# Performance work log

Hardware: AMD Instinct MI355X
Metric: run time of the kernel (lower is better)

## Reference

```python
import jax, jax.numpy as jnp
import numpy as np

B, F_IN, N, S = 2, 128, 192, 192   # batch, in_features, n_nodes, seq (seq==n_nodes required by mask broadcast)
H, D = 4, 64                        # n_heads, n_hidden (out_features = H*D = 256)
NEG_SLOPE = 0.2


def setup_inputs() -> dict:
    key = jax.random.key(0)
    ks = jax.random.split(key, 6)
    X = jax.random.normal(ks[0], (B, F_IN, N, S), dtype=jnp.float32)
    A = jax.random.randint(ks[1], (N, N, 1), 0, 2, dtype=jnp.int32)
    W_lin = jax.random.normal(ks[2], (F_IN, H * D), dtype=jnp.float32) * 0.05
    b_lin = jax.random.uniform(ks[3], (H * D,), dtype=jnp.float32)
    W_attn = jax.random.normal(ks[4], (2 * D,), dtype=jnp.float32) * 0.05
    b_attn = jax.random.uniform(ks[5], (1,), dtype=jnp.float32)
    return {"X": X, "A": A, "W_lin": W_lin, "b_lin": b_lin,
            "W_attn": W_attn, "b_attn": b_attn}


def reference(X, A, W_lin, b_lin, W_attn, b_attn):
    # Dropout is identity (eval mode).
    b, f, n, s = X.shape
    x = jnp.transpose(X, (0, 3, 2, 1))                      # (b, s, n, f)
    g = (x @ W_lin + b_lin).reshape(b, s, n, H, D)          # (b, s, n, H, D)
    # attn is affine: attn(cat[g_i, g_j]) = a_src.g_i + a_dst.g_j + b_attn
    a_src, a_dst = W_attn[:D], W_attn[D:]
    s_src = jnp.einsum('bsnhd,d->bsnh', g, a_src)
    s_dst = jnp.einsum('bsnhd,d->bsnh', g, a_dst)
    e = s_src[:, :, :, None, :] + s_dst[:, :, None, :, :] + b_attn[0]  # (b, s, n_i, n_j, H)
    e = jnp.where(e >= 0, e, NEG_SLOPE * e)                 # LeakyReLU
    # torch masked_fill broadcast: mask (n,n,1,1) aligns with e dims (s, n_i, n_j, H)
    e = jnp.where(A[..., None] == 0, -jnp.inf, e)
    alphas = jax.nn.softmax(e, axis=1)                      # softmax over seq dim (dim=1, as in source)
    alphas = jnp.nan_to_num(alphas, nan=0.0)
    # einsum 'mnojh,klphf->mnohf': independent sums over j (alphas) and k,l,p (g)
    sum_g = g.sum(axis=(0, 1, 2))                           # (H, D)
    attn_res = alphas.sum(axis=3)[..., None] * sum_g        # (b, s, n, H, D)
    out = attn_res.reshape(b, s, n, H * D)                  # concat=True
    return jnp.transpose(out, (0, 3, 2, 1))                 # (b, out_features, n, s)
```

## Files before the change

### kernel.cpp

```cpp
#include <hip/hip_runtime.h>
#include <math.h>

#define B_ 2
#define F_ 128
#define N_ 192
#define S_ 192
#define NS_ (N_ * S_)
#define SLOPE 0.2f
#define LOG2E 1.4426950408889634f
#define NEG_INF (-__builtin_inff())

#if defined(__has_builtin)
#if __has_builtin(__builtin_amdgcn_exp2f)
#define EXP2(x) __builtin_amdgcn_exp2f(x)
#else
#define EXP2(x) exp2f(x)
#endif
#else
#define EXP2(x) exp2f(x)
#endif

#define OFF_WSRC 0
#define OFF_WDST 512
#define OFF_CSRC 1024
#define OFF_CDST 1028
#define OFF_SUMG 1040
#define OFF_PART 1296
#define OFF_PE   2320
#define OFF_QD   (OFF_PE + 8 * NS_ * 2)
#define OFF_QT   (OFF_QD + 8 * NS_ * 2)

__global__ __launch_bounds__(256) void kPre(const float* __restrict__ X,
                                            const float* __restrict__ W_lin,
                                            const float* __restrict__ b_lin,
                                            const float* __restrict__ W_attn,
                                            const float* __restrict__ b_attn,
                                            float* __restrict__ ws) {
    int blk = blockIdx.x, t = threadIdx.x;
    if (blk < 1024) {
        int sq = blk & 3, f = (blk >> 2) & 127, b = blk >> 9;
        const float4* p = (const float4*)(X + ((size_t)(b * F_ + f)) * NS_ + sq * 9216);
        float acc = 0.f;
#pragma unroll
        for (int k = 0; k < 9; k++) {
            float4 v = p[t + k * 256];
            acc += (v.x + v.y) + (v.z + v.w);
        }
        for (int o = 32; o; o >>= 1) acc += __shfl_down(acc, o, 64);
        __shared__ float red[4];
        if ((t & 63) == 0) red[t >> 6] = acc;
        __syncthreads();
        if (t == 0)
            ws[OFF_PART + sq * 256 + b * 128 + f] = (red[0] + red[1]) + (red[2] + red[3]);
    } else if (blk == 1024) {
        const float4* wa = (const float4*)W_attn;
        for (int c = t; c < 512; c += 256) {
            int f = c >> 2, h = c & 3;
            const float4* wl = (const float4*)(W_lin + f * 256 + h * 64);
            float as = 0.f, ad = 0.f;
#pragma unroll
            for (int q = 0; q < 16; q++) {
                float4 w = wl[q], a1 = wa[q], a2 = wa[16 + q];
                as += w.x * a1.x + w.y * a1.y + w.z * a1.z + w.w * a1.w;
                ad += w.x * a2.x + w.y * a2.y + w.z * a2.z + w.w * a2.w;
            }
            ws[OFF_WSRC + c] = as * LOG2E;
            ws[OFF_WDST + c] = ad * LOG2E;
        }
    } else {
        if (t < 4) {
            float c = 0.f;
            for (int d = 0; d < 64; d++) c += b_lin[t * 64 + d] * W_attn[d];
            ws[OFF_CSRC + t] = (c + b_attn[0]) * LOG2E;
        } else if (t < 8) {
            int h = t - 4;
            float c = 0.f;
            for (int d = 0; d < 64; d++) c += b_lin[h * 64 + d] * W_attn[64 + d];
            ws[OFF_CDST + h] = c * LOG2E;
        }
    }
}

__global__ __launch_bounds__(256) void kProj(const float* __restrict__ X,
                                             const int* __restrict__ A,
                                             const float* __restrict__ W_lin,
                                             const float* __restrict__ b_lin,
                                             float* __restrict__ ws) {
    __shared__ float4 wsl[128], wdl[128];
    __shared__ float red[4 * 64 * 9];
    __shared__ float xs[128];
    __shared__ float wbuf[4096];
    int t = threadIdx.x, blk = blockIdx.x;
    if (blk < 1152) {
        int n = blk % 192, bsc = blk / 192;
        int b = bsc / 3, sc = bsc % 3;
        if (t < 128) {
            wsl[t] = ((const float4*)(ws + OFF_WSRC))[t];
            wdl[t] = ((const float4*)(ws + OFF_WDST))[t];
        }
        __syncthreads();
        int fq = t >> 6, lane = t & 63;
        int s = sc * 64 + lane;
        float aS[4] = {0, 0, 0, 0}, aD[4] = {0, 0, 0, 0};
        const float* xp = X + (size_t)(b * F_) * NS_ + n * S_ + s;
        int f0 = fq * 32;
#pragma unroll 8
        for (int fi = 0; fi < 32; fi++) {
            float x = xp[(size_t)(f0 + fi) * NS_];
            float4 w1 = wsl[f0 + fi], w2 = wdl[f0 + fi];
            aS[0] += x * w1.x; aS[1] += x * w1.y; aS[2] += x * w1.z; aS[3] += x * w1.w;
            aD[0] += x * w2.x; aD[1] += x * w2.y; aD[2] += x * w2.z; aD[3] += x * w2.w;
        }
        float* rp = red + t * 9;
#pragma unroll
        for (int h = 0; h < 4; h++) { rp[h] = aS[h]; rp[4 + h] = aD[h]; }
        __syncthreads();
        float2* PEp = (float2*)(ws + OFF_PE);
        float2* QDp = (float2*)(ws + OFF_QD);
        float2* QTp = (float2*)(ws + OFF_QT);
#pragma unroll
        for (int c = t; c < 512; c += 256) {
            int s_loc = c >> 3, k = c & 7;
            float v = red[s_loc * 9 + k] + red[(64 + s_loc) * 9 + k] +
                      red[(128 + s_loc) * 9 + k] + red[(192 + s_loc) * 9 + k];
            int ss = sc * 64 + s_loc;
            if (k < 4) {
                int bh = b * 4 + k;
                bool masked = (A[ss * 192 + n] == 0);
                float2 pr;
                if (masked) { pr.x = 0.f; pr.y = 0.f; }
                else {
                    float pt = v + ws[OFF_CSRC + k];
                    pr.x = EXP2(pt); pr.y = EXP2(0.2f * pt);
                }
                PEp[(size_t)bh * NS_ + n * 192 + ss] = pr;
            } else {
                int h = k - 4, bh = b * 4 + h;
                float dv = v + ws[OFF_CDST + h];
                float2 qr; qr.x = EXP2(dv); qr.y = EXP2(0.2f * dv);
                QDp[(size_t)bh * NS_ + ss * 192 + n] = qr;
                QTp[(size_t)bh * NS_ + n * 192 + ss] = qr;
            }
        }
    } else {
        if (t < 128) {
            float v = 0.f;
#pragma unroll
            for (int q = 0; q < 8; q++) v += ws[OFF_PART + q * 128 + t];
            xs[t] = v;
        }
        float acc = 0.f;
        for (int ch = 0; ch < 8; ch++) {
            const float4* s4 = (const float4*)(W_lin + ch * 4096);
            __syncthreads();
#pragma unroll
            for (int k = 0; k < 4; k++) ((float4*)wbuf)[t + k * 256] = s4[t + k * 256];
            __syncthreads();
#pragma unroll
            for (int fi = 0; fi < 16; fi++) acc += xs[ch * 16 + fi] * wbuf[fi * 256 + t];
        }
        ws[OFF_SUMG + t] = acc + 73728.f * b_lin[t];
    }
}

__global__ __launch_bounds__(384) void kAttn(const float* __restrict__ ws,
                                             float* __restrict__ out) {
    int blk = blockIdx.x, t = threadIdx.x;
    int bh = blk & 7, iq = blk >> 3;
    int b = bh >> 2, h = bh & 3;
    __shared__ float4 pe4[192];
    __shared__ float zpart[768];
    __shared__ float zr_sh[384];
    __shared__ float sg_sh[64];
    const float2* PEp = (const float2*)(ws + OFF_PE) + (size_t)bh * NS_;
    const float2* QDp = (const float2*)(ws + OFF_QD) + (size_t)bh * NS_;
    const float2* QTp = (const float2*)(ws + OFF_QT) + (size_t)bh * NS_;
    if (t < 64) sg_sh[t] = ws[OFF_SUMG + h * 64 + t];
    if (t < 192) {
        float2 a = PEp[(iq * 2) * 192 + t];
        float2 c = PEp[(iq * 2 + 1) * 192 + t];
        pe4[t] = make_float4(a.x, a.y, c.x, c.y);
    }
    __syncthreads();

    {
        int sq = t / 192, j = t - sq * 192;
        float z0 = 0.f, z1 = 0.f;
#pragma unroll 8
        for (int s = sq * 96; s < sq * 96 + 96; s++) {
            float4 E = pe4[s];
            float2 F = QDp[s * 192 + j];
            z0 += fmaxf(E.x * F.x, E.y * F.y);
            z1 += fmaxf(E.z * F.x, E.w * F.y);
        }
        zpart[sq * 384 + j] = z0;
        zpart[sq * 384 + 192 + j] = z1;
    }
    __syncthreads();
    {
        float Z = zpart[t] + zpart[384 + t];
        zr_sh[t] = (Z != 0.f) ? (1.f / Z) : 0.f;
    }
    __syncthreads();

    {
        int i_loc = t / 192, s = t - i_loc * 192;
        float4 E4 = pe4[s];
        float Ex = i_loc ? E4.z : E4.x;
        float Ey = i_loc ? E4.w : E4.y;
        const float* zr = zr_sh + i_loc * 192;
        float acc = 0.f;
#pragma unroll 8
        for (int j = 0; j < 192; j++) {
            float2 G = QTp[j * 192 + s];
            acc += fmaxf(Ex * G.x, Ey * G.y) * zr[j];
        }
        int i = iq * 2 + i_loc;
        float* op = out + (((size_t)(b * 256 + h * 64)) * 192 + i) * 192 + s;
#pragma unroll 8
        for (int d = 0; d < 64; d++)
            op[(size_t)d * NS_] = acc * sg_sh[d];
    }
}

extern "C" void kernel_launch(void* const* d_in, const int* in_sizes, int n_in,
                              void* d_out, int out_size, void* d_ws, size_t ws_size,
                              hipStream_t stream) {
    const float* X      = (const float*)d_in[0];
    const int*   A      = (const int*)d_in[1];
    const float* W_lin  = (const float*)d_in[2];
    const float* b_lin  = (const float*)d_in[3];
    const float* W_attn = (const float*)d_in[4];
    const float* b_attn = (const float*)d_in[5];
    float* out = (float*)d_out;
    float* ws  = (float*)d_ws;

    kPre<<<1026, 256, 0, stream>>>(X, W_lin, b_lin, W_attn, b_attn, ws);
    kProj<<<1153, 256, 0, stream>>>(X, A, W_lin, b_lin, ws);
    kAttn<<<768, 384, 0, stream>>>(ws, out);
}
```

Before: 159.8 us.

## Store raw dst scores and recompute exponentials in attention, three rows per block

```diff
diff --git a/kernel.cpp b/kernel.cpp
--- a/kernel.cpp
+++ b/kernel.cpp
@@ -28,7 +28,7 @@
 #define OFF_PART 1296
 #define OFF_PE   2320
 #define OFF_QD   (OFF_PE + 8 * NS_ * 2)
-#define OFF_QT   (OFF_QD + 8 * NS_ * 2)
+#define OFF_QT   (OFF_QD + 8 * NS_)
 
 __global__ __launch_bounds__(256) void kPre(const float* __restrict__ X,
                                             const float* __restrict__ W_lin,
@@ -116,8 +116,8 @@
         for (int h = 0; h < 4; h++) { rp[h] = aS[h]; rp[4 + h] = aD[h]; }
         __syncthreads();
         float2* PEp = (float2*)(ws + OFF_PE);
-        float2* QDp = (float2*)(ws + OFF_QD);
-        float2* QTp = (float2*)(ws + OFF_QT);
+        float*  QDf = ws + OFF_QD;
+        float*  QTf = ws + OFF_QT;
 #pragma unroll
         for (int c = t; c < 512; c += 256) {
             int s_loc = c >> 3, k = c & 7;
@@ -137,9 +137,8 @@
             } else {
                 int h = k - 4, bh = b * 4 + h;
                 float dv = v + ws[OFF_CDST + h];
-                float2 qr; qr.x = EXP2(dv); qr.y = EXP2(0.2f * dv);
-                QDp[(size_t)bh * NS_ + ss * 192 + n] = qr;
-                QTp[(size_t)bh * NS_ + n * 192 + ss] = qr;
+                QDf[(size_t)bh * NS_ + ss * 192 + n] = dv;
+                QTf[(size_t)bh * NS_ + n * 192 + ss] = dv;
             }
         }
     } else {
@@ -163,59 +162,81 @@
     }
 }
 
-__global__ __launch_bounds__(384) void kAttn(const float* __restrict__ ws,
+__global__ __launch_bounds__(576) void kAttn(const float* __restrict__ ws,
                                              float* __restrict__ out) {
     int blk = blockIdx.x, t = threadIdx.x;
-    int bh = blk & 7, iq = blk >> 3;
+    int bh = blk & 7, it = blk >> 3;
     int b = bh >> 2, h = bh & 3;
-    __shared__ float4 pe4[192];
-    __shared__ float zpart[768];
-    __shared__ float zr_sh[384];
+    __shared__ float4 peA[192];
+    __shared__ float2 peB[192];
+    __shared__ float zpart[3 * 3 * 192];
+    __shared__ float4 zr4[192];
+    __shared__ float accp[3 * 3 * 192];
     __shared__ float sg_sh[64];
     const float2* PEp = (const float2*)(ws + OFF_PE) + (size_t)bh * NS_;
-    const float2* QDp = (const float2*)(ws + OFF_QD) + (size_t)bh * NS_;
-    const float2* QTp = (const float2*)(ws + OFF_QT) + (size_t)bh * NS_;
+    const float*  QDf = ws + OFF_QD + (size_t)bh * NS_;
+    const float*  QTf = ws + OFF_QT + (size_t)bh * NS_;
     if (t < 64) sg_sh[t] = ws[OFF_SUMG + h * 64 + t];
     if (t < 192) {
-        float2 a = PEp[(iq * 2) * 192 + t];
-        float2 c = PEp[(iq * 2 + 1) * 192 + t];
-        pe4[t] = make_float4(a.x, a.y, c.x, c.y);
+        float2 e0 = PEp[(it * 3 + 0) * 192 + t];
+        float2 e1 = PEp[(it * 3 + 1) * 192 + t];
+        float2 e2 = PEp[(it * 3 + 2) * 192 + t];
+        peA[t] = make_float4(e0.x, e0.y, e1.x, e1.y);
+        peB[t] = e2;
     }
     __syncthreads();
 
     {
         int sq = t / 192, j = t - sq * 192;
-        float z0 = 0.f, z1 = 0.f;
-#pragma unroll 8
-        for (int s = sq * 96; s < sq * 96 + 96; s++) {
-            float4 E = pe4[s];
-            float2 F = QDp[s * 192 + j];
-            z0 += fmaxf(E.x * F.x, E.y * F.y);
-            z1 += fmaxf(E.z * F.x, E.w * F.y);
-        }
-        zpart[sq * 384 + j] = z0;
-        zpart[sq * 384 + 192 + j] = z1;
-    }
-    __syncthreads();
-    {
-        float Z = zpart[t] + zpart[384 + t];
-        zr_sh[t] = (Z != 0.f) ? (1.f / Z) : 0.f;
-    }
-    __syncthreads();
-
-    {
-        int i_loc = t / 192, s = t - i_loc * 192;
-        float4 E4 = pe4[s];
-        float Ex = i_loc ? E4.z : E4.x;
-        float Ey = i_loc ? E4.w : E4.y;
-        const float* zr = zr_sh + i_loc * 192;
-        float acc = 0.f;
-#pragma unroll 8
-        for (int j = 0; j < 192; j++) {
-            float2 G = QTp[j * 192 + s];
-            acc += fmaxf(Ex * G.x, Ey * G.y) * zr[j];
-        }
-        int i = iq * 2 + i_loc;
+        float z0 = 0.f, z1 = 0.f, z2 = 0.f;
+#pragma unroll 8
+        for (int s = sq * 64; s < sq * 64 + 64; s++) {
+            float q = QDf[s * 192 + j];
+            float Q1 = EXP2(q), Q2 = EXP2(0.2f * q);
+            float4 Ea = peA[s];
+            float2 Eb = peB[s];
+            z0 += fmaxf(Ea.x * Q1, Ea.y * Q2);
+            z1 += fmaxf(Ea.z * Q1, Ea.w * Q2);
+            z2 += fmaxf(Eb.x * Q1, Eb.y * Q2);
+        }
+        zpart[sq * 576 + 0 * 192 + j] = z0;
+        zpart[sq * 576 + 1 * 192 + j] = z1;
+        zpart[sq * 576 + 2 * 192 + j] = z2;
+    }
+    __syncthreads();
+    {
+        int r = t / 192, j = t - r * 192;
+        float Z = zpart[r * 192 + j] + zpart[576 + r * 192 + j] +
+                  zpart[1152 + r * 192 + j];
+        ((float*)zr4)[j * 4 + r] = (Z != 0.f) ? (1.f / Z) : 0.f;
+    }
+    __syncthreads();
+
+    {
+        int jt = t / 192, s = t - jt * 192;
+        float4 Ea = peA[s];
+        float2 Eb = peB[s];
+        float a0 = 0.f, a1 = 0.f, a2 = 0.f;
+#pragma unroll 8
+        for (int j = jt * 64; j < jt * 64 + 64; j++) {
+            float g = QTf[j * 192 + s];
+            float G1 = EXP2(g), G2 = EXP2(0.2f * g);
+            float4 Z4 = zr4[j];
+            a0 += fmaxf(Ea.x * G1, Ea.y * G2) * Z4.x;
+            a1 += fmaxf(Ea.z * G1, Ea.w * G2) * Z4.y;
+            a2 += fmaxf(Eb.x * G1, Eb.y * G2) * Z4.z;
+        }
+        accp[jt * 576 + 0 * 192 + s] = a0;
+        accp[jt * 576 + 1 * 192 + s] = a1;
+        accp[jt * 576 + 2 * 192 + s] = a2;
+    }
+    __syncthreads();
+
+    {
+        int r = t / 192, s = t - r * 192;
+        float acc = accp[r * 192 + s] + accp[576 + r * 192 + s] +
+                    accp[1152 + r * 192 + s];
+        int i = it * 3 + r;
         float* op = out + (((size_t)(b * 256 + h * 64)) * 192 + i) * 192 + s;
 #pragma unroll 8
         for (int d = 0; d < 64; d++)
@@ -237,5 +258,5 @@
 
     kPre<<<1026, 256, 0, stream>>>(X, W_lin, b_lin, W_attn, b_attn, ws);
     kProj<<<1153, 256, 0, stream>>>(X, A, W_lin, b_lin, ws);
-    kAttn<<<768, 384, 0, stream>>>(ws, out);
-}
+    kAttn<<<512, 576, 0, stream>>>(ws, out);
+}
```

After: 163.9 us. 1.03x slower.
